# Kernel optimization log

Hardware: AMD Instinct MI355X
Metric: run time of the kernel (lower is better)

The kernel has to match this reference:

```python
import jax, jax.numpy as jnp
import numpy as np

N_NODES = 8      # 4 regions + 4 boundaries
N_STEPS = 3


def _step_graph(nodes, Wd, Ws, b):
    """One all-pairs message-passing step.

    nodes: [N, B, C, H, W]
    Wd:    [N, C, C]  receiver-i conv weight acting on (nodes[j] - nodes[i])
    Ws:    [N, C, C]  receiver-i conv weight acting on nodes[i]
    b:     [N, C]
    edges[j][i] = Wd_i @ (nodes[j]-nodes[i]) + Ws_i @ nodes[i] + b_i   (1x1 conv)
    out[i] = sum_{j != i} relu(edges[j][i]) * nodes[j] + nodes[i]
    """
    # receiver-dependent self term: [N(i), B, C, H, W]
    self_term = jnp.einsum('iod,ibdhw->ibohw', Ws, nodes) + b[:, None, :, None, None]
    # pairwise differences nodes[j] - nodes[i]: [N(j), N(i), B, C, H, W]
    diff = nodes[:, None] - nodes[None, :]
    e = jnp.einsum('iod,jibdhw->jibohw', Wd, diff) + self_term[None]
    gate = jax.nn.relu(e)
    # zero out the diagonal (i == j contributes nothing)
    mask = (1.0 - jnp.eye(N_NODES, dtype=nodes.dtype))[:, :, None, None, None, None]
    gate = gate * mask
    # message[i] = sum_j gate[j,i] * nodes[j]
    msg = jnp.einsum('jibchw,jbchw->ibchw', gate, nodes)
    return msg + nodes


def setup_inputs() -> dict:
    key = jax.random.key(0)
    k1, k2, k3 = jax.random.split(key, 3)
    B, C, H, W = 4, 32, 96, 96
    nodes = jax.random.normal(k1, (N_NODES, B, C, H, W), dtype=jnp.float32)
    # 1x1 conv weights [N, C_out, 2C_in]; scaled ~1/(2C) to keep 3 steps numerically tame
    W_edge = jax.random.normal(k2, (N_NODES, C, 2 * C), dtype=jnp.float32) * 0.05
    b_edge = jax.random.normal(k3, (N_NODES, C), dtype=jnp.float32) * 0.05
    return {"nodes": nodes, "W_edge": W_edge, "b_edge": b_edge}


def reference(nodes, W_edge, b_edge):
    C = nodes.shape[2]
    Wd = W_edge[:, :, :C]   # acts on nodes[j] - nodes[i]
    Ws = W_edge[:, :, C:]   # acts on nodes[i]
    for _ in range(N_STEPS):
        nodes = _step_graph(nodes, Wd, Ws, b_edge)
    return nodes  # [N, B, C, H, W]; first half = regions, second half = boundaries
```

## Files before the change

### kernel.cpp

```cpp
#include <hip/hip_runtime.h>
#include <hip/hip_bf16.h>


#define NN 8
#define NSTEPS 3
#define BB 4
#define CC 32
#define HWSZ 9216
#define PX 16
#define CPF 36
#define CPS 40

typedef __bf16 bf16x8 __attribute__((ext_vector_type(8)));
typedef __bf16 bf16x4 __attribute__((ext_vector_type(4)));
typedef float f32x4 __attribute__((ext_vector_type(4)));

#define MFMA(A, B, C) __builtin_amdgcn_mfma_f32_16x16x32_bf16((A), (B), (C), 0, 0, 0)

__device__ __forceinline__ void split3(float v, __bf16& h, __bf16& m, __bf16& l) {
    h = (__bf16)v;
    float r1 = v - (float)h;
    m = (__bf16)r1;
    l = (__bf16)(r1 - (float)m);
}

__global__ __launch_bounds__(256, 2)
void gcn3_mfma(const float* __restrict__ nodes,
               const float* __restrict__ we,
               const float* __restrict__ be,
               float* __restrict__ out) {
    __shared__ float  xf[NN][PX][CPF];
    __shared__ __bf16 xs[3][NN][PX][CPS];

    const int tid  = threadIdx.x;
    const int wid  = tid >> 6;
    const int lane = tid & 63;
    const int col  = lane & 15;
    const int quad = lane >> 4;

    const int irec[2] = { wid, wid + 4 };

    bf16x8 awd[2][2][3];
    bf16x8 awsd[2][2][3];
    f32x4  bias[2][2];
    #pragma unroll
    for (int r = 0; r < 2; ++r) {
        #pragma unroll
        for (int t = 0; t < 2; ++t) {
            const float* wp = we + (size_t)(irec[r] * CC + 16 * t + col) * (2 * CC) + quad * 8;
            f32x4 wd0 = *(const f32x4*)(wp);
            f32x4 wd1 = *(const f32x4*)(wp + 4);
            f32x4 ws0 = *(const f32x4*)(wp + CC);
            f32x4 ws1 = *(const f32x4*)(wp + CC + 4);
            #pragma unroll
            for (int k = 0; k < 8; ++k) {
                float d = (k < 4) ? wd0[k & 3] : wd1[k & 3];
                float s = (k < 4) ? ws0[k & 3] : ws1[k & 3];
                __bf16 h, m, l;
                split3(d, h, m, l);
                awd[r][t][0][k] = h; awd[r][t][1][k] = m; awd[r][t][2][k] = l;
                split3(s - d, h, m, l);
                awsd[r][t][0][k] = h; awsd[r][t][1][k] = m; awsd[r][t][2][k] = l;
            }
            #pragma unroll
            for (int k = 0; k < 4; ++k)
                bias[r][t][k] = be[irec[r] * CC + 16 * t + quad * 4 + k];
        }
    }

    const int q0  = blockIdx.x * PX;
    const int b   = q0 / HWSZ;
    const int hw0 = q0 - b * HWSZ;

    #pragma unroll
    for (int kk = 0; kk < 4; ++kk) {
        int idx = tid + kk * 256;
        int p4  = (idx & 3) * 4;
        int c   = (idx >> 2) & 31;
        int n   = idx >> 7;
        f32x4 v = *(const f32x4*)(nodes + (size_t)((n * BB + b) * CC + c) * HWSZ + hw0 + p4);
        #pragma unroll
        for (int e = 0; e < 4; ++e) {
            float x = v[e];
            xf[n][p4 + e][c] = x;
            __bf16 h, m, l;
            split3(x, h, m, l);
            xs[0][n][p4 + e][c] = h;
            xs[1][n][p4 + e][c] = m;
            xs[2][n][p4 + e][c] = l;
        }
    }
    __syncthreads();

    #pragma unroll 1
    for (int step = 0; step < NSTEPS; ++step) {
        f32x4 qf[2][2];
        #pragma unroll
        for (int r = 0; r < 2; ++r) {
            bf16x8 bq[3];
            #pragma unroll
            for (int s = 0; s < 3; ++s)
                bq[s] = *(const bf16x8*)&xs[s][irec[r]][col][quad * 8];
            #pragma unroll
            for (int t = 0; t < 2; ++t) {
                f32x4 acc = bias[r][t];
                acc = MFMA(awsd[r][t][0], bq[0], acc);
                acc = MFMA(awsd[r][t][0], bq[1], acc);
                acc = MFMA(awsd[r][t][1], bq[0], acc);
                acc = MFMA(awsd[r][t][0], bq[2], acc);
                acc = MFMA(awsd[r][t][2], bq[0], acc);
                acc = MFMA(awsd[r][t][1], bq[1], acc);
                qf[r][t] = acc;
            }
        }
        f32x4 msg[2][2];
        #pragma unroll
        for (int r = 0; r < 2; ++r)
            #pragma unroll
            for (int t = 0; t < 2; ++t)
                msg[r][t] = *(const f32x4*)&xf[irec[r]][col][16 * t + quad * 4];

        #pragma unroll
        for (int j = 0; j < NN; ++j) {
            bf16x8 bj[3];
            #pragma unroll
            for (int s = 0; s < 3; ++s)
                bj[s] = *(const bf16x8*)&xs[s][j][col][quad * 8];
            f32x4 xg[2];
            #pragma unroll
            for (int t = 0; t < 2; ++t)
                xg[t] = *(const f32x4*)&xf[j][col][16 * t + quad * 4];
            #pragma unroll
            for (int r = 0; r < 2; ++r) {
                const bool diag = (j == irec[r]);
                #pragma unroll
                for (int t = 0; t < 2; ++t) {
                    f32x4 e = qf[r][t];
                    e = MFMA(awd[r][t][0], bj[0], e);
                    e = MFMA(awd[r][t][0], bj[1], e);
                    e = MFMA(awd[r][t][1], bj[0], e);
                    e = MFMA(awd[r][t][0], bj[2], e);
                    e = MFMA(awd[r][t][2], bj[0], e);
                    e = MFMA(awd[r][t][1], bj[1], e);
                    #pragma unroll
                    for (int k = 0; k < 4; ++k) {
                        float g = diag ? 0.0f : fmaxf(e[k], 0.0f);
                        msg[r][t][k] = fmaf(g, xg[t][k], msg[r][t][k]);
                    }
                }
            }
        }
        __syncthreads();
        #pragma unroll
        for (int r = 0; r < 2; ++r) {
            #pragma unroll
            for (int t = 0; t < 2; ++t) {
                *(f32x4*)&xf[irec[r]][col][16 * t + quad * 4] = msg[r][t];
                bf16x4 h4, m4, l4;
                #pragma unroll
                for (int k = 0; k < 4; ++k) {
                    __bf16 h, m, l;
                    split3(msg[r][t][k], h, m, l);
                    h4[k] = h; m4[k] = m; l4[k] = l;
                }
                *(bf16x4*)&xs[0][irec[r]][col][16 * t + quad * 4] = h4;
                *(bf16x4*)&xs[1][irec[r]][col][16 * t + quad * 4] = m4;
                *(bf16x4*)&xs[2][irec[r]][col][16 * t + quad * 4] = l4;
            }
        }
        __syncthreads();
    }

    #pragma unroll
    for (int kk = 0; kk < 4; ++kk) {
        int idx = tid + kk * 256;
        int p4  = (idx & 3) * 4;
        int c   = (idx >> 2) & 31;
        int n   = idx >> 7;
        f32x4 v;
        #pragma unroll
        for (int e = 0; e < 4; ++e) v[e] = xf[n][p4 + e][c];
        *(f32x4*)(out + (size_t)((n * BB + b) * CC + c) * HWSZ + hw0 + p4) = v;
    }
}

extern "C" void kernel_launch(void* const* d_in, const int* in_sizes, int n_in,
                              void* d_out, int out_size, void* d_ws, size_t ws_size,
                              hipStream_t stream) {
    const float* nodes  = (const float*)d_in[0];
    const float* W_edge = (const float*)d_in[1];
    const float* b_edge = (const float*)d_in[2];
    float* outp = (float*)d_out;

    dim3 grid((BB * HWSZ) / PX);
    dim3 block(256);
    gcn3_mfma<<<grid, block, 0, stream>>>(nodes, W_edge, b_edge, outp);
}
```

Before: 160.9 us.

## Drop fp32 LDS copy, recompute self weights per step, raise occupancy

Removes the fp32 shared-memory copy of node features and rebuilds fp32 values by summing the three bf16 split parts. The self-term weights and bias are now reloaded and re-split from global memory each step instead of held in registers, which frees VGPRs so launch bounds can allow 3 blocks per CU. The diagonal term is branched out so it skips its MFMAs, the last step's LDS writeback and barrier are dropped, and results are stored straight from registers to global memory. The cost is extra global loads and split work each step, and output stores that are less coalesced (16 consecutive floats per row).

```diff
diff --git a/kernel.cpp b/kernel.cpp
--- a/kernel.cpp
+++ b/kernel.cpp
@@ -8,12 +8,13 @@
 #define CC 32
 #define HWSZ 9216
 #define PX 16
-#define CPF 36
 #define CPS 40
 
 typedef __bf16 bf16x8 __attribute__((ext_vector_type(8)));
 typedef __bf16 bf16x4 __attribute__((ext_vector_type(4)));
-typedef float f32x4 __attribute__((ext_vector_type(4)));
+typedef __bf16 bf16x2 __attribute__((ext_vector_type(2)));
+typedef float  f32x4  __attribute__((ext_vector_type(4)));
+typedef float  f32x2  __attribute__((ext_vector_type(2)));
 
 #define MFMA(A, B, C) __builtin_amdgcn_mfma_f32_16x16x32_bf16((A), (B), (C), 0, 0, 0)
 
@@ -24,12 +25,11 @@
     l = (__bf16)(r1 - (float)m);
 }
 
-__global__ __launch_bounds__(256, 2)
-void gcn3_mfma(const float* __restrict__ nodes,
-               const float* __restrict__ we,
-               const float* __restrict__ be,
-               float* __restrict__ out) {
-    __shared__ float  xf[NN][PX][CPF];
+__global__ __launch_bounds__(256, 3)
+void gcn3_mfma2(const float* __restrict__ nodes,
+                const float* __restrict__ we,
+                const float* __restrict__ be,
+                float* __restrict__ out) {
     __shared__ __bf16 xs[3][NN][PX][CPS];
 
     const int tid  = threadIdx.x;
@@ -38,33 +38,22 @@
     const int col  = lane & 15;
     const int quad = lane >> 4;
 
-    const int irec[2] = { wid, wid + 4 };
-
     bf16x8 awd[2][2][3];
-    bf16x8 awsd[2][2][3];
-    f32x4  bias[2][2];
     #pragma unroll
     for (int r = 0; r < 2; ++r) {
+        const int ir = wid + 4 * r;
         #pragma unroll
         for (int t = 0; t < 2; ++t) {
-            const float* wp = we + (size_t)(irec[r] * CC + 16 * t + col) * (2 * CC) + quad * 8;
-            f32x4 wd0 = *(const f32x4*)(wp);
-            f32x4 wd1 = *(const f32x4*)(wp + 4);
-            f32x4 ws0 = *(const f32x4*)(wp + CC);
-            f32x4 ws1 = *(const f32x4*)(wp + CC + 4);
+            const float* wp = we + (size_t)((ir * CC + 16 * t + col) * (2 * CC)) + quad * 8;
+            f32x4 w0 = *(const f32x4*)wp;
+            f32x4 w1 = *(const f32x4*)(wp + 4);
             #pragma unroll
             for (int k = 0; k < 8; ++k) {
-                float d = (k < 4) ? wd0[k & 3] : wd1[k & 3];
-                float s = (k < 4) ? ws0[k & 3] : ws1[k & 3];
+                float d = (k < 4) ? w0[k & 3] : w1[k & 3];
                 __bf16 h, m, l;
                 split3(d, h, m, l);
                 awd[r][t][0][k] = h; awd[r][t][1][k] = m; awd[r][t][2][k] = l;
-                split3(s - d, h, m, l);
-                awsd[r][t][0][k] = h; awsd[r][t][1][k] = m; awsd[r][t][2][k] = l;
-            }
-            #pragma unroll
-            for (int k = 0; k < 4; ++k)
-                bias[r][t][k] = be[irec[r] * CC + 16 * t + quad * 4 + k];
+            }
         }
     }
 
@@ -75,112 +64,144 @@
     #pragma unroll
     for (int kk = 0; kk < 4; ++kk) {
         int idx = tid + kk * 256;
-        int p4  = (idx & 3) * 4;
-        int c   = (idx >> 2) & 31;
-        int n   = idx >> 7;
-        f32x4 v = *(const f32x4*)(nodes + (size_t)((n * BB + b) * CC + c) * HWSZ + hw0 + p4);
-        #pragma unroll
-        for (int e = 0; e < 4; ++e) {
-            float x = v[e];
-            xf[n][p4 + e][c] = x;
-            __bf16 h, m, l;
-            split3(x, h, m, l);
-            xs[0][n][p4 + e][c] = h;
-            xs[1][n][p4 + e][c] = m;
-            xs[2][n][p4 + e][c] = l;
+        int p2 = (idx & 7) * 2;
+        int c2 = ((idx >> 3) & 15) * 2;
+        int n  = idx >> 7;
+        const float* gp = nodes + (size_t)((n * BB + b) * CC + c2) * HWSZ + hw0 + p2;
+        f32x2 v0 = *(const f32x2*)gp;
+        f32x2 v1 = *(const f32x2*)(gp + HWSZ);
+        #pragma unroll
+        for (int e = 0; e < 2; ++e) {
+            __bf16 h0, m0, l0, h1, m1, l1;
+            split3(v0[e], h0, m0, l0);
+            split3(v1[e], h1, m1, l1);
+            *(bf16x2*)&xs[0][n][p2 + e][c2] = bf16x2{h0, h1};
+            *(bf16x2*)&xs[1][n][p2 + e][c2] = bf16x2{m0, m1};
+            *(bf16x2*)&xs[2][n][p2 + e][c2] = bf16x2{l0, l1};
         }
     }
     __syncthreads();
+
+    f32x4 msg[2][2];
 
     #pragma unroll 1
     for (int step = 0; step < NSTEPS; ++step) {
+        asm volatile("" ::: "memory");
+
         f32x4 qf[2][2];
         #pragma unroll
         for (int r = 0; r < 2; ++r) {
-            bf16x8 bq[3];
-            #pragma unroll
-            for (int s = 0; s < 3; ++s)
-                bq[s] = *(const bf16x8*)&xs[s][irec[r]][col][quad * 8];
+            const int ir = wid + 4 * r;
+            bf16x8 bq0 = *(const bf16x8*)&xs[0][ir][col][quad * 8];
+            bf16x8 bq1 = *(const bf16x8*)&xs[1][ir][col][quad * 8];
+            bf16x8 bq2 = *(const bf16x8*)&xs[2][ir][col][quad * 8];
             #pragma unroll
             for (int t = 0; t < 2; ++t) {
-                f32x4 acc = bias[r][t];
-                acc = MFMA(awsd[r][t][0], bq[0], acc);
-                acc = MFMA(awsd[r][t][0], bq[1], acc);
-                acc = MFMA(awsd[r][t][1], bq[0], acc);
-                acc = MFMA(awsd[r][t][0], bq[2], acc);
-                acc = MFMA(awsd[r][t][2], bq[0], acc);
-                acc = MFMA(awsd[r][t][1], bq[1], acc);
+                const float* wp = we + (size_t)((ir * CC + 16 * t + col) * (2 * CC)) + quad * 8;
+                f32x4 d0 = *(const f32x4*)wp;
+                f32x4 d1 = *(const f32x4*)(wp + 4);
+                f32x4 s0 = *(const f32x4*)(wp + CC);
+                f32x4 s1 = *(const f32x4*)(wp + CC + 4);
+                bf16x8 ah, am, al;
+                #pragma unroll
+                for (int k = 0; k < 8; ++k) {
+                    float sv = ((k < 4) ? s0[k & 3] : s1[k & 3]) - ((k < 4) ? d0[k & 3] : d1[k & 3]);
+                    __bf16 h, m, l;
+                    split3(sv, h, m, l);
+                    ah[k] = h; am[k] = m; al[k] = l;
+                }
+                f32x4 acc = *(const f32x4*)(be + ir * CC + 16 * t + quad * 4);
+                acc = MFMA(ah, bq0, acc);
+                acc = MFMA(ah, bq1, acc);
+                acc = MFMA(am, bq0, acc);
+                acc = MFMA(ah, bq2, acc);
+                acc = MFMA(al, bq0, acc);
+                acc = MFMA(am, bq1, acc);
                 qf[r][t] = acc;
             }
         }
-        f32x4 msg[2][2];
+
         #pragma unroll
         for (int r = 0; r < 2; ++r)
             #pragma unroll
             for (int t = 0; t < 2; ++t)
-                msg[r][t] = *(const f32x4*)&xf[irec[r]][col][16 * t + quad * 4];
+                msg[r][t] = f32x4{0.f, 0.f, 0.f, 0.f};
 
         #pragma unroll
         for (int j = 0; j < NN; ++j) {
-            bf16x8 bj[3];
-            #pragma unroll
-            for (int s = 0; s < 3; ++s)
-                bj[s] = *(const bf16x8*)&xs[s][j][col][quad * 8];
+            bf16x8 bj0 = *(const bf16x8*)&xs[0][j][col][quad * 8];
+            bf16x8 bj1 = *(const bf16x8*)&xs[1][j][col][quad * 8];
+            bf16x8 bj2 = *(const bf16x8*)&xs[2][j][col][quad * 8];
             f32x4 xg[2];
             #pragma unroll
-            for (int t = 0; t < 2; ++t)
-                xg[t] = *(const f32x4*)&xf[j][col][16 * t + quad * 4];
+            for (int t = 0; t < 2; ++t) {
+                bf16x4 h4 = *(const bf16x4*)&xs[0][j][col][16 * t + quad * 4];
+                bf16x4 m4 = *(const bf16x4*)&xs[1][j][col][16 * t + quad * 4];
+                bf16x4 l4 = *(const bf16x4*)&xs[2][j][col][16 * t + quad * 4];
+                #pragma unroll
+                for (int k = 0; k < 4; ++k)
+                    xg[t][k] = (float)h4[k] + (float)m4[k] + (float)l4[k];
+            }
             #pragma unroll
             for (int r = 0; r < 2; ++r) {
-                const bool diag = (j == irec[r]);
+                const int ir = wid + 4 * r;
+                if (j == ir) {
+                    #pragma unroll
+                    for (int t = 0; t < 2; ++t)
+                        #pragma unroll
+                        for (int k = 0; k < 4; ++k)
+                            msg[r][t][k] += xg[t][k];
+                } else {
+                    #pragma unroll
+                    for (int t = 0; t < 2; ++t) {
+                        f32x4 e = qf[r][t];
+                        e = MFMA(awd[r][t][0], bj0, e);
+                        e = MFMA(awd[r][t][0], bj1, e);
+                        e = MFMA(awd[r][t][1], bj0, e);
+                        e = MFMA(awd[r][t][0], bj2, e);
+                        e = MFMA(awd[r][t][2], bj0, e);
+                        e = MFMA(awd[r][t][1], bj1, e);
+                        #pragma unroll
+                        for (int k = 0; k < 4; ++k)
+                            msg[r][t][k] = fmaf(fmaxf(e[k], 0.f), xg[t][k], msg[r][t][k]);
+                    }
+                }
+            }
+        }
+
+        if (step < NSTEPS - 1) {
+            __syncthreads();
+            #pragma unroll
+            for (int r = 0; r < 2; ++r) {
+                const int ir = wid + 4 * r;
                 #pragma unroll
                 for (int t = 0; t < 2; ++t) {
-                    f32x4 e = qf[r][t];
-                    e = MFMA(awd[r][t][0], bj[0], e);
-                    e = MFMA(awd[r][t][0], bj[1], e);
-                    e = MFMA(awd[r][t][1], bj[0], e);
-                    e = MFMA(awd[r][t][0], bj[2], e);
-                    e = MFMA(awd[r][t][2], bj[0], e);
-                    e = MFMA(awd[r][t][1], bj[1], e);
+                    bf16x4 h4, m4, l4;
                     #pragma unroll
                     for (int k = 0; k < 4; ++k) {
-                        float g = diag ? 0.0f : fmaxf(e[k], 0.0f);
-                        msg[r][t][k] = fmaf(g, xg[t][k], msg[r][t][k]);
+                        __bf16 h, m, l;
+                        split3(msg[r][t][k], h, m, l);
+                        h4[k] = h; m4[k] = m; l4[k] = l;
                     }
+                    *(bf16x4*)&xs[0][ir][col][16 * t + quad * 4] = h4;
+                    *(bf16x4*)&xs[1][ir][col][16 * t + quad * 4] = m4;
+                    *(bf16x4*)&xs[2][ir][col][16 * t + quad * 4] = l4;
                 }
             }
-        }
-        __syncthreads();
-        #pragma unroll
-        for (int r = 0; r < 2; ++r) {
-            #pragma unroll
-            for (int t = 0; t < 2; ++t) {
-                *(f32x4*)&xf[irec[r]][col][16 * t + quad * 4] = msg[r][t];
-                bf16x4 h4, m4, l4;
-                #pragma unroll
-                for (int k = 0; k < 4; ++k) {
-                    __bf16 h, m, l;
-                    split3(msg[r][t][k], h, m, l);
-                    h4[k] = h; m4[k] = m; l4[k] = l;
-                }
-                *(bf16x4*)&xs[0][irec[r]][col][16 * t + quad * 4] = h4;
-                *(bf16x4*)&xs[1][irec[r]][col][16 * t + quad * 4] = m4;
-                *(bf16x4*)&xs[2][irec[r]][col][16 * t + quad * 4] = l4;
-            }
-        }
-        __syncthreads();
+            __syncthreads();
+        }
     }
 
     #pragma unroll
-    for (int kk = 0; kk < 4; ++kk) {
-        int idx = tid + kk * 256;
-        int p4  = (idx & 3) * 4;
-        int c   = (idx >> 2) & 31;
-        int n   = idx >> 7;
-        f32x4 v;
-        #pragma unroll
-        for (int e = 0; e < 4; ++e) v[e] = xf[n][p4 + e][c];
-        *(f32x4*)(out + (size_t)((n * BB + b) * CC + c) * HWSZ + hw0 + p4) = v;
+    for (int r = 0; r < 2; ++r) {
+        const int ir = wid + 4 * r;
+        #pragma unroll
+        for (int t = 0; t < 2; ++t) {
+            float* op = out + (size_t)((ir * BB + b) * CC + 16 * t + quad * 4) * HWSZ + hw0 + col;
+            #pragma unroll
+            for (int k = 0; k < 4; ++k)
+                op[(size_t)k * HWSZ] = msg[r][t][k];
+        }
     }
 }
 
@@ -194,5 +215,5 @@
 
     dim3 grid((BB * HWSZ) / PX);
     dim3 block(256);
-    gcn3_mfma<<<grid, block, 0, stream>>>(nodes, W_edge, b_edge, outp);
+    gcn3_mfma2<<<grid, block, 0, stream>>>(nodes, W_edge, b_edge, outp);
 }
```

Result: slower. 214.4 us (+33.3%).
